# Kernel tuning notes

Hardware: AMD Instinct MI355X
Metric: run time of the kernel (lower is better)

The kernel has to match this reference:

```python
import jax, jax.numpy as jnp
import numpy as np

INPUT_DIM = 1024
NUM_HEADS = 16
D_K = 1024
HEAD_DIM = D_K // NUM_HEADS


def setup_inputs() -> dict:
    key = jax.random.key(0)
    ks = jax.random.split(key, 9)
    s_in = 1.0 / np.sqrt(INPUT_DIM)
    s_dk = 1.0 / np.sqrt(D_K)
    return {
        "x": jax.random.normal(ks[0], (2, 2048, INPUT_DIM), dtype=jnp.float32),
        "Wq": jax.random.uniform(ks[1], (INPUT_DIM, D_K), minval=-s_in, maxval=s_in, dtype=jnp.float32),
        "bq": jax.random.uniform(ks[2], (D_K,), minval=-s_in, maxval=s_in, dtype=jnp.float32),
        "Wk": jax.random.uniform(ks[3], (INPUT_DIM, D_K), minval=-s_in, maxval=s_in, dtype=jnp.float32),
        "bk": jax.random.uniform(ks[4], (D_K,), minval=-s_in, maxval=s_in, dtype=jnp.float32),
        "Wv": jax.random.uniform(ks[5], (INPUT_DIM, D_K), minval=-s_in, maxval=s_in, dtype=jnp.float32),
        "bv": jax.random.uniform(ks[6], (D_K,), minval=-s_in, maxval=s_in, dtype=jnp.float32),
        "Wo": jax.random.uniform(ks[7], (D_K, INPUT_DIM), minval=-s_dk, maxval=s_dk, dtype=jnp.float32),
        "bo": jax.random.uniform(ks[8], (INPUT_DIM,), minval=-s_dk, maxval=s_dk, dtype=jnp.float32),
    }


def reference(x, Wq, bq, Wk, bk, Wv, bv, Wo, bo):
    B, S, _ = x.shape
    H, D = NUM_HEADS, HEAD_DIM
    # QKV projections -> [B, H, S, D]
    q = (x @ Wq + bq).reshape(B, S, H, D).transpose(0, 2, 1, 3)
    k = (x @ Wk + bk).reshape(B, S, H, D).transpose(0, 2, 1, 3)
    v = (x @ Wv + bv).reshape(B, S, H, D).transpose(0, 2, 1, 3)
    scores = jnp.einsum("bhsd,bhtd->bhst", q, k) / jnp.sqrt(jnp.asarray(D, x.dtype))
    attn = jax.nn.softmax(scores, axis=-1)
    out = jnp.einsum("bhst,bhtd->bhsd", attn, v)  # [B,H,S,D]
    out = out.transpose(0, 2, 1, 3).reshape(B, S, H * D)
    return out @ Wo + bo
```

## Files before the change

### kernel.cpp

```cpp
#include <hip/hip_runtime.h>
#include <stdint.h>

typedef _Float16 f16;
typedef f16 f16x4 __attribute__((ext_vector_type(4)));
typedef f16 f16x8 __attribute__((ext_vector_type(8)));
typedef __fp16 hf16x2 __attribute__((ext_vector_type(2)));
typedef float f32x4 __attribute__((ext_vector_type(4)));
typedef float f32x16 __attribute__((ext_vector_type(16)));

#define AS1 __attribute__((address_space(1)))
#define AS3 __attribute__((address_space(3)))

__device__ __forceinline__ void gll16(const void* g, void* l) {
  __builtin_amdgcn_global_load_lds((AS1 void*)g, (AS3 void*)l, 16, 0, 0);
}

__device__ __forceinline__ f32x4 mfma16(f16x8 a, f16x8 b, f32x4 c) {
  return __builtin_amdgcn_mfma_f32_16x16x32_f16(a, b, c, 0, 0, 0);
}
__device__ __forceinline__ f32x16 mfma32(f16x8 a, f16x8 b, f32x16 c) {
  return __builtin_amdgcn_mfma_f32_32x32x16_f16(a, b, c, 0, 0, 0);
}

__device__ __forceinline__ uint32_t pkrtz(float a, float b) {
  union { hf16x2 h; uint32_t u; } c;
  c.h = __builtin_amdgcn_cvt_pkrtz(a, b);
  return c.u;
}

__device__ __forceinline__ void pl32(uint32_t& x, uint32_t& y) {
  asm("v_permlane32_swap_b32 %0, %1" : "+v"(x), "+v"(y));
}

__device__ __forceinline__ f16x8 mk_bfrag(float e0, float e1, float e2, float e3,
                                          float e4, float e5, float e6, float e7) {
  uint32_t x0 = pkrtz(e0, e1), y0 = pkrtz(e4, e5);
  uint32_t x1 = pkrtz(e2, e3), y1 = pkrtz(e6, e7);
  pl32(x0, y0);
  pl32(x1, y1);
  union { uint32_t w[4]; f16x8 v; } u;
  u.w[0] = x0; u.w[1] = x1; u.w[2] = y0; u.w[3] = y1;
  return u.v;
}

__device__ __forceinline__ f32x16 zero16() {
  f32x16 z;
#pragma unroll
  for (int i = 0; i < 16; i++) z[i] = 0.f;
  return z;
}


__global__ __launch_bounds__(256) void pack_x_k(const float* __restrict__ x,
                                                f16* __restrict__ xh, int n) {
  int i = (blockIdx.x * 256 + threadIdx.x) * 8;
  if (i < n) {
    float4 a = *(const float4*)(x + i);
    float4 b = *(const float4*)(x + i + 4);
    f16x8 o;
    o[0] = (f16)a.x; o[1] = (f16)a.y; o[2] = (f16)a.z; o[3] = (f16)a.w;
    o[4] = (f16)b.x; o[5] = (f16)b.y; o[6] = (f16)b.z; o[7] = (f16)b.w;
    *(f16x8*)(xh + i) = o;
  }
}

__global__ __launch_bounds__(256) void pack_w_k(const float* __restrict__ Wq,
                                                const float* __restrict__ Wk,
                                                const float* __restrict__ Wv,
                                                const float* __restrict__ Wo,
                                                f16* __restrict__ Wt) {
  __shared__ f16 t[64][65];
  const float* W = (blockIdx.z == 0) ? Wq : (blockIdx.z == 1) ? Wk
                   : (blockIdx.z == 2) ? Wv : Wo;
  int n0 = blockIdx.x * 64, k0 = blockIdx.y * 64;
  int tid = threadIdx.x;
  int kr = tid >> 4;
  int nc = (tid & 15) * 4;
#pragma unroll
  for (int i = 0; i < 4; i++) {
    int k = k0 + kr + i * 16;
    float4 w = *(const float4*)(W + (size_t)k * 1024 + n0 + nc);
    t[nc + 0][kr + i * 16] = (f16)w.x;
    t[nc + 1][kr + i * 16] = (f16)w.y;
    t[nc + 2][kr + i * 16] = (f16)w.z;
    t[nc + 3][kr + i * 16] = (f16)w.w;
  }
  __syncthreads();
  int nr = tid >> 2;
  int c0 = (tid & 3) * 16;
  alignas(16) f16 tmp[16];
#pragma unroll
  for (int e = 0; e < 16; e++) tmp[e] = t[nr][c0 + e];
  f16* dst = Wt + (size_t)(blockIdx.z * 1024 + n0 + nr) * 1024 + k0 + c0;
  *(f16x8*)(dst) = *(const f16x8*)(tmp);
  *(f16x8*)(dst + 8) = *(const f16x8*)(tmp + 8);
}

__device__ __forceinline__ void gemm_main(const f16* __restrict__ A,
                                          const f16* __restrict__ B,
                                          int m0, int n0,
                                          f16* Al, f16* Bl,
                                          f32x4 acc[4][4]) {
  const int K = 1024;
  int tid = threadIdx.x;
  int lane = tid & 63, wid = tid >> 6;
  int wr = (wid >> 1) * 64, wc = (wid & 1) * 64;
#pragma unroll
  for (int mi = 0; mi < 4; mi++)
#pragma unroll
    for (int nj = 0; nj < 4; nj++) {
      f32x4 z = {0.f, 0.f, 0.f, 0.f};
      acc[mi][nj] = z;
    }
  int srow = lane >> 3;
  int sgr = (lane & 7) ^ srow;
  int lr = lane & 15, lg = lane >> 4;
  for (int kt = 0; kt < 16; ++kt) {
    __syncthreads();
#pragma unroll
    for (int q = 0; q < 4; q++) {
      int chunk = wid * 4 + q;
      int row = chunk * 8 + srow;
      gll16(A + (size_t)(m0 + row) * K + kt * 64 + sgr * 8, Al + chunk * 512);
      gll16(B + (size_t)(n0 + row) * K + kt * 64 + sgr * 8, Bl + chunk * 512);
    }
    __syncthreads();
#pragma unroll
    for (int kk = 0; kk < 2; kk++) {
      f16x8 af[4], bf[4];
#pragma unroll
      for (int mi = 0; mi < 4; mi++) {
        int row = wr + mi * 16 + lr;
        int gr = (kk * 4 + lg) ^ (row & 7);
        af[mi] = *(const f16x8*)(Al + row * 64 + gr * 8);
      }
#pragma unroll
      for (int nj = 0; nj < 4; nj++) {
        int row = wc + nj * 16 + lr;
        int gr = (kk * 4 + lg) ^ (row & 7);
        bf[nj] = *(const f16x8*)(Bl + row * 64 + gr * 8);
      }
#pragma unroll
      for (int mi = 0; mi < 4; mi++)
#pragma unroll
        for (int nj = 0; nj < 4; nj++)
          acc[mi][nj] = mfma16(af[mi], bf[nj], acc[mi][nj]);
    }
  }
}

__global__ __launch_bounds__(256) void gemm_qkv_k(const f16* __restrict__ Xh,
                                                  const f16* __restrict__ Wt,
                                                  const float* __restrict__ bq,
                                                  const float* __restrict__ bk,
                                                  const float* __restrict__ bv,
                                                  f16* __restrict__ Q,
                                                  f16* __restrict__ Kb,
                                                  f16* __restrict__ Vt) {
  __shared__ f16 Al[128 * 64];
  __shared__ f16 Bl[128 * 64];
  f32x4 acc[4][4];
  int m0 = blockIdx.y * 128, n0 = blockIdx.x * 128;
  gemm_main(Xh, Wt, m0, n0, Al, Bl, acc);

  int lane = threadIdx.x & 63, wid = threadIdx.x >> 6;
  int wr = (wid >> 1) * 64, wc = (wid & 1) * 64;
  int lg = lane >> 4, lc = lane & 15;
  int which = n0 >> 10;
  if (which == 2) {
#pragma unroll
    for (int mi = 0; mi < 4; mi++)
#pragma unroll
      for (int nj = 0; nj < 4; nj++) {
        int nh = (n0 + wc + nj * 16 + lc) & 1023;
        int h = nh >> 6, d = nh & 63;
        float bb = bv[nh];
        int mbase = m0 + wr + mi * 16 + lg * 4;
        int b = mbase >> 11, s = mbase & 2047;
        f16x4 vv;
#pragma unroll
        for (int r = 0; r < 4; r++) vv[r] = (f16)(acc[mi][nj][r] + bb);
        *(f16x4*)(Vt + ((size_t)(b * 16 + h) * 64 + d) * 2048 + s) = vv;
      }
  } else {
    const float* bias = (which == 0) ? bq : bk;
    f16* out = (which == 0) ? Q : Kb;
    float scale = (which == 0) ? 0.125f : 1.0f;
#pragma unroll
    for (int mi = 0; mi < 4; mi++)
#pragma unroll
      for (int nj = 0; nj < 4; nj++) {
        int nh = (n0 + wc + nj * 16 + lc) & 1023;
        int h = nh >> 6, d = nh & 63;
        float bb = bias[nh];
#pragma unroll
        for (int r = 0; r < 4; r++) {
          int m = m0 + wr + mi * 16 + lg * 4 + r;
          int b = m >> 11, s = m & 2047;
          float v = (acc[mi][nj][r] + bb) * scale;
          out[((size_t)(b * 16 + h) * 2048 + s) * 64 + d] = (f16)v;
        }
      }
  }
}

__global__ __launch_bounds__(256) void gemm_out_k(const f16* __restrict__ Oh,
                                                  const f16* __restrict__ Wt,
                                                  const float* __restrict__ bo,
                                                  float* __restrict__ out) {
  __shared__ f16 Al[128 * 64];
  __shared__ f16 Bl[128 * 64];
  f32x4 acc[4][4];
  int m0 = blockIdx.y * 128, n0 = blockIdx.x * 128;
  gemm_main(Oh, Wt, m0, n0, Al, Bl, acc);

  int lane = threadIdx.x & 63, wid = threadIdx.x >> 6;
  int wr = (wid >> 1) * 64, wc = (wid & 1) * 64;
  int lg = lane >> 4, lc = lane & 15;
#pragma unroll
  for (int mi = 0; mi < 4; mi++)
#pragma unroll
    for (int nj = 0; nj < 4; nj++) {
      int n = n0 + wc + nj * 16 + lc;
      float bb = bo[n];
#pragma unroll
      for (int r = 0; r < 4; r++) {
        int m = m0 + wr + mi * 16 + lg * 4 + r;
        out[(size_t)m * 1024 + n] = acc[mi][nj][r] + bb;
      }
    }
}

__global__ __launch_bounds__(128) void attn_k(const f16* __restrict__ Q,
                                              const f16* __restrict__ K,
                                              const f16* __restrict__ Vt,
                                              f16* __restrict__ Oh) {
  __shared__ alignas(16) f16 Kl[2][64 * 64];
  __shared__ alignas(16) f16 Vl[2][64 * 64];

  int tid = threadIdx.x, lane = tid & 63, wid = tid >> 6;
  int q5 = lane & 31, hi = lane >> 5;
  int b0 = blockIdx.x;
  int qc = (b0 >> 3) & 31;
  int bh = (b0 & 7) + ((b0 >> 8) << 3);
  int q0w = qc * 64 + wid * 32;

  const f16* Qp = Q + (size_t)bh * 2048 * 64;
  const f16* Kp = K + (size_t)bh * 2048 * 64;
  const f16* Vp = Vt + (size_t)bh * 64 * 2048;

  f16x8 qf0, qf1, qf2, qf3;
  {
    const f16* qr = Qp + (size_t)(q0w + q5) * 64 + hi * 8;
    qf0 = *(const f16x8*)(qr);
    qf1 = *(const f16x8*)(qr + 16);
    qf2 = *(const f16x8*)(qr + 32);
    qf3 = *(const f16x8*)(qr + 48);
  }

  f32x16 o0 = zero16(), o1 = zero16();
  float m = -1e30f, lsum = 0.f;

  int srow = lane >> 3;
  int sg8 = ((lane & 7) ^ srow) * 8;

  auto STAGE = [&](int buf, int t0) {
#pragma unroll
    for (int qi = 0; qi < 4; qi++) {
      int chunk = wid * 4 + qi;
      int row = chunk * 8 + srow;
      gll16(Kp + (size_t)(t0 + row) * 64 + sg8, &Kl[buf][chunk * 512]);
      gll16(Vp + (size_t)row * 2048 + t0 + sg8, &Vl[buf][chunk * 512]);
    }
  };

  STAGE(0, 0);

  int r0 = q5, r1 = 32 + q5;
  int sw0 = (r0 & 7), sw1 = (r1 & 7);

  for (int t = 0; t < 32; ++t) {
    int cur = t & 1;
    if (t < 31) {
      STAGE(cur ^ 1, (t + 1) * 64);
      asm volatile("s_waitcnt vmcnt(8)" ::: "memory");
    } else {
      asm volatile("s_waitcnt vmcnt(0)" ::: "memory");
    }
    __builtin_amdgcn_s_barrier();

    const f16* kb = Kl[cur];
    const f16* vb = Vl[cur];

    f32x16 s0 = zero16(), s1 = zero16();
#pragma unroll
    for (int ks = 0; ks < 4; ks++) {
      int g = 2 * ks + hi;
      f16x8 k0 = *(const f16x8*)(kb + r0 * 64 + ((g ^ sw0) << 3));
      f16x8 k1 = *(const f16x8*)(kb + r1 * 64 + ((g ^ sw1) << 3));
      f16x8 qv = (ks == 0) ? qf0 : (ks == 1) ? qf1 : (ks == 2) ? qf2 : qf3;
      s0 = mfma32(k0, qv, s0);
      s1 = mfma32(k1, qv, s1);
    }

    float mx = s0[0];
#pragma unroll
    for (int i = 1; i < 16; i++) mx = fmaxf(mx, s0[i]);
#pragma unroll
    for (int i = 0; i < 16; i++) mx = fmaxf(mx, s1[i]);
    mx = fmaxf(mx, __shfl_xor(mx, 32));
    float mn = fmaxf(m, mx);
    float al = __expf(m - mn);
    m = mn;
    float sum = 0.f;
#pragma unroll
    for (int i = 0; i < 16; i++) { s0[i] = __expf(s0[i] - mn); sum += s0[i]; }
#pragma unroll
    for (int i = 0; i < 16; i++) { s1[i] = __expf(s1[i] - mn); sum += s1[i]; }
    sum += __shfl_xor(sum, 32);
    lsum = lsum * al + sum;
#pragma unroll
    for (int i = 0; i < 16; i++) { o0[i] *= al; o1[i] *= al; }

    f16x8 pb0 = mk_bfrag(s0[0], s0[1], s0[2], s0[3], s0[4], s0[5], s0[6], s0[7]);
    f16x8 pb1 = mk_bfrag(s0[8], s0[9], s0[10], s0[11], s0[12], s0[13], s0[14], s0[15]);
    f16x8 pb2 = mk_bfrag(s1[0], s1[1], s1[2], s1[3], s1[4], s1[5], s1[6], s1[7]);
    f16x8 pb3 = mk_bfrag(s1[8], s1[9], s1[10], s1[11], s1[12], s1[13], s1[14], s1[15]);

#pragma unroll
    for (int ks = 0; ks < 4; ks++) {
      int g = 2 * ks + hi;
      f16x8 v0 = *(const f16x8*)(vb + r0 * 64 + ((g ^ sw0) << 3));
      f16x8 v1 = *(const f16x8*)(vb + r1 * 64 + ((g ^ sw1) << 3));
      f16x8 pv = (ks == 0) ? pb0 : (ks == 1) ? pb1 : (ks == 2) ? pb2 : pb3;
      o0 = mfma32(v0, pv, o0);
      o1 = mfma32(v1, pv, o1);
    }

    asm volatile("" ::: "memory");
    __builtin_amdgcn_s_barrier();
  }

  float inv = 1.f / lsum;
  int b = bh >> 4, h = bh & 15;
  f16* op = Oh + ((size_t)(b * 2048 + q0w + q5)) * 1024 + h * 64;
#pragma unroll
  for (int qd = 0; qd < 4; qd++) {
    f16x4 w0, w1;
#pragma unroll
    for (int j = 0; j < 4; j++) {
      int r = qd * 4 + j;
      w0[j] = (f16)(o0[r] * inv);
      w1[j] = (f16)(o1[r] * inv);
    }
    int d0 = 8 * qd + 4 * hi;
    *(f16x4*)(op + d0) = w0;
    *(f16x4*)(op + 32 + d0) = w1;
  }
}


extern "C" void kernel_launch(void* const* d_in, const int* in_sizes, int n_in,
                              void* d_out, int out_size, void* d_ws, size_t ws_size,
                              hipStream_t stream) {
  const float* x  = (const float*)d_in[0];
  const float* Wq = (const float*)d_in[1];
  const float* bq = (const float*)d_in[2];
  const float* Wk = (const float*)d_in[3];
  const float* bk = (const float*)d_in[4];
  const float* Wv = (const float*)d_in[5];
  const float* bv = (const float*)d_in[6];
  const float* Wo = (const float*)d_in[7];
  const float* bo = (const float*)d_in[8];
  float* out = (float*)d_out;

  char* ws = (char*)d_ws;
  const size_t MB8 = (size_t)8 << 20;
  f16* Xh = (f16*)(ws + 0 * MB8);
  f16* Wt = (f16*)(ws + 1 * MB8);
  f16* Q  = (f16*)(ws + 2 * MB8);
  f16* Kb = (f16*)(ws + 3 * MB8);
  f16* Vt = (f16*)(ws + 4 * MB8);
  f16* Oh = (f16*)(ws + 5 * MB8);

  pack_x_k<<<dim3(2048), dim3(256), 0, stream>>>(x, Xh, 4096 * 1024);
  pack_w_k<<<dim3(16, 16, 4), dim3(256), 0, stream>>>(Wq, Wk, Wv, Wo, Wt);
  gemm_qkv_k<<<dim3(24, 32), dim3(256), 0, stream>>>(Xh, Wt, bq, bk, bv, Q, Kb, Vt);
  attn_k<<<dim3(1024), dim3(128), 0, stream>>>(Q, Kb, Vt, Oh);
  gemm_out_k<<<dim3(8, 32), dim3(256), 0, stream>>>(Oh, Wt + (size_t)3072 * 1024, bo, out);
}
```

Before: 145.3 us.

## Use exp2 softmax with log2e-folded scale, lazy rescale, early V loads, setprio

```diff
diff --git a/kernel.cpp b/kernel.cpp
--- a/kernel.cpp
+++ b/kernel.cpp
@@ -4,7 +4,6 @@
 typedef _Float16 f16;
 typedef f16 f16x4 __attribute__((ext_vector_type(4)));
 typedef f16 f16x8 __attribute__((ext_vector_type(8)));
-typedef __fp16 hf16x2 __attribute__((ext_vector_type(2)));
 typedef float f32x4 __attribute__((ext_vector_type(4)));
 typedef float f32x16 __attribute__((ext_vector_type(16)));
 
@@ -22,9 +21,10 @@
   return __builtin_amdgcn_mfma_f32_32x32x16_f16(a, b, c, 0, 0, 0);
 }
 
-__device__ __forceinline__ uint32_t pkrtz(float a, float b) {
-  union { hf16x2 h; uint32_t u; } c;
-  c.h = __builtin_amdgcn_cvt_pkrtz(a, b);
+__device__ __forceinline__ uint32_t pk_rtn(float a, float b) {
+  union { f16 h[2]; uint32_t u; } c;
+  c.h[0] = (f16)a;
+  c.h[1] = (f16)b;
   return c.u;
 }
 
@@ -34,8 +34,8 @@
 
 __device__ __forceinline__ f16x8 mk_bfrag(float e0, float e1, float e2, float e3,
                                           float e4, float e5, float e6, float e7) {
-  uint32_t x0 = pkrtz(e0, e1), y0 = pkrtz(e4, e5);
-  uint32_t x1 = pkrtz(e2, e3), y1 = pkrtz(e6, e7);
+  uint32_t x0 = pk_rtn(e0, e1), y0 = pk_rtn(e4, e5);
+  uint32_t x1 = pk_rtn(e2, e3), y1 = pk_rtn(e6, e7);
   pl32(x0, y0);
   pl32(x1, y1);
   union { uint32_t w[4]; f16x8 v; } u;
@@ -185,7 +185,7 @@
   } else {
     const float* bias = (which == 0) ? bq : bk;
     f16* out = (which == 0) ? Q : Kb;
-    float scale = (which == 0) ? 0.125f : 1.0f;
+    float scale = (which == 0) ? 0.1803368801111204f : 1.0f;
 #pragma unroll
     for (int mi = 0; mi < 4; mi++)
 #pragma unroll
@@ -277,7 +277,7 @@
   STAGE(0, 0);
 
   int r0 = q5, r1 = 32 + q5;
-  int sw0 = (r0 & 7), sw1 = (r1 & 7);
+  int sw = q5 & 7;
 
   for (int t = 0; t < 32; ++t) {
     int cur = t & 1;
@@ -293,49 +293,76 @@
     const f16* vb = Vl[cur];
 
     f32x16 s0 = zero16(), s1 = zero16();
+    __builtin_amdgcn_s_setprio(1);
 #pragma unroll
     for (int ks = 0; ks < 4; ks++) {
       int g = 2 * ks + hi;
-      f16x8 k0 = *(const f16x8*)(kb + r0 * 64 + ((g ^ sw0) << 3));
-      f16x8 k1 = *(const f16x8*)(kb + r1 * 64 + ((g ^ sw1) << 3));
+      f16x8 k0 = *(const f16x8*)(kb + r0 * 64 + ((g ^ sw) << 3));
+      f16x8 k1 = *(const f16x8*)(kb + r1 * 64 + ((g ^ sw) << 3));
       f16x8 qv = (ks == 0) ? qf0 : (ks == 1) ? qf1 : (ks == 2) ? qf2 : qf3;
       s0 = mfma32(k0, qv, s0);
       s1 = mfma32(k1, qv, s1);
     }
-
-    float mx = s0[0];
-#pragma unroll
-    for (int i = 1; i < 16; i++) mx = fmaxf(mx, s0[i]);
-#pragma unroll
-    for (int i = 0; i < 16; i++) mx = fmaxf(mx, s1[i]);
+    __builtin_amdgcn_s_setprio(0);
+
+    f16x8 vf0[4], vf1[4];
+#pragma unroll
+    for (int ks = 0; ks < 4; ks++) {
+      int g = 2 * ks + hi;
+      vf0[ks] = *(const f16x8*)(vb + r0 * 64 + ((g ^ sw) << 3));
+      vf1[ks] = *(const f16x8*)(vb + r1 * 64 + ((g ^ sw) << 3));
+    }
+
+    float w[16];
+#pragma unroll
+    for (int i = 0; i < 16; i++) w[i] = fmaxf(s0[i], s1[i]);
+#pragma unroll
+    for (int st = 8; st > 0; st >>= 1)
+#pragma unroll
+      for (int i = 0; i < st; i++) w[i] = fmaxf(w[i], w[i + st]);
+    float mx = w[0];
     mx = fmaxf(mx, __shfl_xor(mx, 32));
-    float mn = fmaxf(m, mx);
-    float al = __expf(m - mn);
-    m = mn;
-    float sum = 0.f;
-#pragma unroll
-    for (int i = 0; i < 16; i++) { s0[i] = __expf(s0[i] - mn); sum += s0[i]; }
-#pragma unroll
-    for (int i = 0; i < 16; i++) { s1[i] = __expf(s1[i] - mn); sum += s1[i]; }
+
+    if (__any(mx > m)) {
+      float mn = fmaxf(m, mx);
+      float al = __builtin_amdgcn_exp2f(m - mn);
+      m = mn;
+      lsum *= al;
+#pragma unroll
+      for (int i = 0; i < 16; i++) { o0[i] *= al; o1[i] *= al; }
+    }
+    float su0 = 0.f, su1 = 0.f, su2 = 0.f, su3 = 0.f;
+#pragma unroll
+    for (int i = 0; i < 16; i += 4) {
+      s0[i + 0] = __builtin_amdgcn_exp2f(s0[i + 0] - m); su0 += s0[i + 0];
+      s0[i + 1] = __builtin_amdgcn_exp2f(s0[i + 1] - m); su1 += s0[i + 1];
+      s0[i + 2] = __builtin_amdgcn_exp2f(s0[i + 2] - m); su2 += s0[i + 2];
+      s0[i + 3] = __builtin_amdgcn_exp2f(s0[i + 3] - m); su3 += s0[i + 3];
+    }
+#pragma unroll
+    for (int i = 0; i < 16; i += 4) {
+      s1[i + 0] = __builtin_amdgcn_exp2f(s1[i + 0] - m); su0 += s1[i + 0];
+      s1[i + 1] = __builtin_amdgcn_exp2f(s1[i + 1] - m); su1 += s1[i + 1];
+      s1[i + 2] = __builtin_amdgcn_exp2f(s1[i + 2] - m); su2 += s1[i + 2];
+      s1[i + 3] = __builtin_amdgcn_exp2f(s1[i + 3] - m); su3 += s1[i + 3];
+    }
+    float sum = (su0 + su1) + (su2 + su3);
     sum += __shfl_xor(sum, 32);
-    lsum = lsum * al + sum;
-#pragma unroll
-    for (int i = 0; i < 16; i++) { o0[i] *= al; o1[i] *= al; }
+    lsum += sum;
 
     f16x8 pb0 = mk_bfrag(s0[0], s0[1], s0[2], s0[3], s0[4], s0[5], s0[6], s0[7]);
     f16x8 pb1 = mk_bfrag(s0[8], s0[9], s0[10], s0[11], s0[12], s0[13], s0[14], s0[15]);
     f16x8 pb2 = mk_bfrag(s1[0], s1[1], s1[2], s1[3], s1[4], s1[5], s1[6], s1[7]);
     f16x8 pb3 = mk_bfrag(s1[8], s1[9], s1[10], s1[11], s1[12], s1[13], s1[14], s1[15]);
 
+    __builtin_amdgcn_s_setprio(1);
 #pragma unroll
     for (int ks = 0; ks < 4; ks++) {
-      int g = 2 * ks + hi;
-      f16x8 v0 = *(const f16x8*)(vb + r0 * 64 + ((g ^ sw0) << 3));
-      f16x8 v1 = *(const f16x8*)(vb + r1 * 64 + ((g ^ sw1) << 3));
       f16x8 pv = (ks == 0) ? pb0 : (ks == 1) ? pb1 : (ks == 2) ? pb2 : pb3;
-      o0 = mfma32(v0, pv, o0);
-      o1 = mfma32(v1, pv, o1);
-    }
+      o0 = mfma32(vf0[ks], pv, o0);
+      o1 = mfma32(vf1[ks], pv, o1);
+    }
+    __builtin_amdgcn_s_setprio(0);
 
     asm volatile("" ::: "memory");
     __builtin_amdgcn_s_barrier();
```

Result: slower. 149.6 us (+2.9%).
